# Kernel optimization log

Measured on AMD Instinct MI355X. Metric: run time of the kernel, lower is better.

## Reference

```python
import jax, jax.numpy as jnp
import numpy as np

HEAD_SIZE = 128
BLOCK_SIZE = 2048


def setup_inputs() -> dict:
    key = jax.random.key(0)
    k1, k2 = jax.random.split(key)
    B, T, D = 8, 2048, 1024
    x = jax.random.normal(k1, (B, T, D), dtype=jnp.float32)
    # Linear(dim, 3*head_size, bias=False): weight [3*head_size, dim], applied as x @ W.T
    W_qkv = jax.random.normal(k2, (3 * HEAD_SIZE, D), dtype=jnp.float32) * (1.0 / np.sqrt(D))
    return {"x": x, "W_qkv": W_qkv}


def reference(x, W_qkv):
    B, T, D = x.shape
    qkv = jnp.einsum('btd,hd->bth', x, W_qkv)  # [B, T, 3*head_size]
    q = qkv[:, :, :HEAD_SIZE]
    k = qkv[:, :, HEAD_SIZE:2 * HEAD_SIZE]
    v = qkv[:, :, 2 * HEAD_SIZE:]
    scale = 1.0 / np.sqrt(HEAD_SIZE).astype(np.float32)
    score = jnp.einsum('bqh,bkh->bqk', q, k) * scale  # [B, T, T]
    causal = jnp.tril(jnp.ones((T, T), dtype=bool))
    score = jnp.where(causal, score, -jnp.inf)
    attn = jax.nn.softmax(score, axis=-1)
    # dropout p=0.0 (eval) -> identity
    return jnp.einsum('bqk,bkh->bqh', attn, v)  # [B, T, head_size]
```

## Files before the change

kernel.cpp:

```cpp
#include <hip/hip_runtime.h>
#include <hip/hip_bf16.h>
#include <math.h>

#define D_MODEL 1024
#define TLEN    2048

typedef __attribute__((ext_vector_type(8))) short short8;
typedef __attribute__((ext_vector_type(4))) float f32x4;

static __device__ __forceinline__ unsigned short f2bf(float f) {
    __hip_bfloat16 h = __float2bfloat16(f);
    return __builtin_bit_cast(unsigned short, h);
}
static __device__ __forceinline__ float bf2f(unsigned short u) {
    unsigned int x = ((unsigned int)u) << 16;
    return __builtin_bit_cast(float, x);
}
static __device__ __forceinline__ void lds_cp16(void* lds, const void* g) {
    __builtin_amdgcn_global_load_lds(
        (const __attribute__((address_space(1))) unsigned int*)g,
        (__attribute__((address_space(3))) unsigned int*)lds, 16, 0, 0);
}

__global__ __launch_bounds__(256) void pack_w(const float* __restrict__ W,
                                              unsigned short* __restrict__ wt) {
    const int id = blockIdx.x * 256 + threadIdx.x;
    const int h  = id >> 7;
    const int kg = id & 127;
    const int k0 = kg * 8;
    const int kt = k0 >> 6;
    const int kin = k0 & 63;
    const float4 a = *(const float4*)&W[(size_t)h * D_MODEL + k0];
    const float4 b = *(const float4*)&W[(size_t)h * D_MODEL + k0 + 4];
    short8 v;
    v[0] = (short)f2bf(a.x); v[1] = (short)f2bf(a.y);
    v[2] = (short)f2bf(a.z); v[3] = (short)f2bf(a.w);
    v[4] = (short)f2bf(b.x); v[5] = (short)f2bf(b.y);
    v[6] = (short)f2bf(b.z); v[7] = (short)f2bf(b.w);
    const size_t dst = ((size_t)kt * 384 + h) * 64 + (kin ^ ((h & 7) * 8));
    *(short8*)&wt[dst] = v;
}

__global__ __launch_bounds__(256, 2) void qkv_gemm(const float* __restrict__ x,
                                                   const unsigned short* __restrict__ wt,
                                                   unsigned short* __restrict__ qk,
                                                   unsigned short* __restrict__ vt) {
    __shared__ unsigned short As[32 * 64];
    __shared__ unsigned short Bs[384 * 64];

    const int tid  = threadIdx.x;
    const int lane = tid & 63;
    const int w    = tid >> 6;
    const int cc   = lane & 15, g = lane >> 4;
    const int row0 = blockIdx.x * 32;

    const int xr  = tid >> 3;
    const int xg  = tid & 7;

    const f32x4 zero = {0.f, 0.f, 0.f, 0.f};
    f32x4 acc[2][6];
#pragma unroll
    for (int i = 0; i < 2; ++i)
#pragma unroll
        for (int j = 0; j < 6; ++j) acc[i][j] = zero;

    const float* xrow = x + (size_t)(row0 + xr) * D_MODEL + xg * 8;
    float4 xa0 = *(const float4*)(xrow);
    float4 xa1 = *(const float4*)(xrow + 4);

    const unsigned short* wsrc0 = wt + w * 6144 + lane * 8;
    unsigned short* bdst = Bs + w * 6144;

    const int aw = xr * 64 + ((xg ^ (xr & 7)) << 3);

    for (int kt = 0; kt < 16; ++kt) {
        __syncthreads();
        {
            short8 s0;
            s0[0] = (short)f2bf(xa0.x); s0[1] = (short)f2bf(xa0.y);
            s0[2] = (short)f2bf(xa0.z); s0[3] = (short)f2bf(xa0.w);
            s0[4] = (short)f2bf(xa1.x); s0[5] = (short)f2bf(xa1.y);
            s0[6] = (short)f2bf(xa1.z); s0[7] = (short)f2bf(xa1.w);
            *(short8*)&As[aw] = s0;
        }
        const unsigned short* wtk = wsrc0 + (size_t)kt * 24576;
#pragma unroll
        for (int i = 0; i < 12; ++i)
            lds_cp16(bdst + i * 512, wtk + i * 512);
        __syncthreads();

        short8 af[2][2], bf[2][6];
#pragma unroll
        for (int ks = 0; ks < 2; ++ks) {
#pragma unroll
            for (int mt = 0; mt < 2; ++mt) {
                const int row = mt * 16 + cc;
                af[ks][mt] = *(const short8*)&As[row * 64 + (((ks * 4 + g) ^ (row & 7)) << 3)];
            }
#pragma unroll
            for (int nt = 0; nt < 6; ++nt) {
                const int h = w * 96 + nt * 16 + cc;
                bf[ks][nt] = *(const short8*)&Bs[h * 64 + (((ks * 4 + g) ^ (h & 7)) << 3)];
            }
        }
        if (kt + 1 < 16) {
            xa0 = *(const float4*)(xrow + (kt + 1) * 64);
            xa1 = *(const float4*)(xrow + (kt + 1) * 64 + 4);
        }
        __builtin_amdgcn_s_setprio(1);
#pragma unroll
        for (int ks = 0; ks < 2; ++ks)
#pragma unroll
            for (int mt = 0; mt < 2; ++mt)
#pragma unroll
                for (int nt = 0; nt < 6; ++nt)
                    acc[mt][nt] = __builtin_amdgcn_mfma_f32_16x16x32_bf16(
                        af[ks][mt], bf[ks][nt], acc[mt][nt], 0, 0, 0);
        __builtin_amdgcn_s_setprio(0);
    }

    const int bb  = row0 >> 11;
    const int tr0 = row0 & 2047;
#pragma unroll
    for (int mt = 0; mt < 2; ++mt)
#pragma unroll
        for (int nt = 0; nt < 6; ++nt) {
            const int h = w * 96 + nt * 16 + cc;
            if (h < 256) {
                const float qs = (h < 128) ? 0.08838834764831845f : 1.0f;
#pragma unroll
                for (int r = 0; r < 4; ++r) {
                    const int row = row0 + mt * 16 + g * 4 + r;
                    qk[(size_t)row * 256 + h] = f2bf(acc[mt][nt][r] * qs);
                }
            } else {
                const int d    = h - 256;
                const int trow = tr0 + mt * 16 + g * 4;
                ushort4 u;
                u.x = f2bf(acc[mt][nt][0]);
                u.y = f2bf(acc[mt][nt][1]);
                u.z = f2bf(acc[mt][nt][2]);
                u.w = f2bf(acc[mt][nt][3]);
                *(ushort4*)&vt[((size_t)(bb * 128 + d)) * TLEN + trow] = u;
            }
        }
}

__global__ __launch_bounds__(256, 3) void attn_part(const unsigned short* __restrict__ qk,
                                                    const unsigned short* __restrict__ vt,
                                                    unsigned short* __restrict__ po,
                                                    float2* __restrict__ ml) {
    __shared__ unsigned short Ks[64 * 128];
    __shared__ unsigned short Vs[128 * 64];
    __shared__ unsigned short Ps[4][16][72];

    const int tid  = threadIdx.x;
    const int lane = tid & 63;
    const int w    = tid >> 6;
    const int cc   = lane & 15, g = lane >> 4;
    const int bx   = blockIdx.x;
    const int qt   = 31 - (bx / 3);
    const int ggg  = bx % 3;
    const int b    = blockIdx.y;
    const int q0   = qt * 64;
    const int slot = (b * 32 + qt) * 3 + ggg;
    const int n    = qt + 1;
    const int cnt  = (n > ggg) ? ((n - ggg + 2) / 3) : 0;

    if (cnt == 0) {
#pragma unroll
        for (int nt = 0; nt < 8; ++nt)
#pragma unroll
            for (int r = 0; r < 4; ++r)
                po[((size_t)slot * 64 + w * 16 + g * 4 + r) * 128 + nt * 16 + cc] = 0;
        if (g == 0) ml[slot * 64 + w * 16 + cc] = make_float2(-INFINITY, 0.f);
        return;
    }

    short8 qf[4];
    {
        const unsigned short* qb =
            qk + ((size_t)(b * TLEN + q0 + w * 16 + cc)) * 256 + g * 8;
#pragma unroll
        for (int kt = 0; kt < 4; ++kt) qf[kt] = *(const short8*)(qb + kt * 32);
    }

    const f32x4 zero = {0.f, 0.f, 0.f, 0.f};
    f32x4 o[8];
#pragma unroll
    for (int nt = 0; nt < 8; ++nt) o[nt] = zero;
    float mrun = -INFINITY, lrun = 0.f;

    int koff[4], voff[2];
#pragma unroll
    for (int kt = 0; kt < 4; ++kt)
        koff[kt] = cc * 128 + (((kt * 4 + g) ^ (cc & 7)) << 3);
#pragma unroll
    for (int ks = 0; ks < 2; ++ks)
        voff[ks] = cc * 64 + (((ks * 4 + g) ^ (cc & 7)) << 3);

    const int kRow = tid >> 2;
    const int kG0  = (tid & 3) * 4;
    const int vRow = tid >> 1;
    const int vG0  = (tid & 1) * 4;
    const unsigned short* kgp = qk + ((size_t)(b * TLEN + kRow)) * 256 + 128 + kG0 * 8;
    const unsigned short* vgp = vt + ((size_t)(b * 128 + vRow)) * TLEN + vG0 * 8;

    short8 kr[4], vr[4];
#pragma unroll
    for (int i = 0; i < 4; ++i) kr[i] = *(const short8*)(kgp + (size_t)ggg * 16384 + i * 8);
#pragma unroll
    for (int i = 0; i < 4; ++i) vr[i] = *(const short8*)(vgp + ggg * 64 + i * 8);

    for (int s = 0; s < cnt; ++s) {
        const int t  = 3 * s + ggg;
        const int j0 = t * 64;
        __syncthreads();
#pragma unroll
        for (int i = 0; i < 4; ++i) {
            *(short8*)&Ks[kRow * 128 + (((kG0 + i) ^ (kRow & 7)) << 3)] = kr[i];
            *(short8*)&Vs[vRow * 64  + (((vG0 + i) ^ (vRow & 7)) << 3)] = vr[i];
        }
        __syncthreads();
        if (s + 1 < cnt) {
            const int tn = t + 3;
#pragma unroll
            for (int i = 0; i < 4; ++i) kr[i] = *(const short8*)(kgp + (size_t)tn * 16384 + i * 8);
#pragma unroll
            for (int i = 0; i < 4; ++i) vr[i] = *(const short8*)(vgp + tn * 64 + i * 8);
        }

        f32x4 st[4];
#pragma unroll
        for (int jt = 0; jt < 4; ++jt) st[jt] = zero;
        __builtin_amdgcn_s_setprio(1);
#pragma unroll
        for (int kt = 0; kt < 4; ++kt)
#pragma unroll
            for (int jt = 0; jt < 4; ++jt) {
                const short8 kf = *(const short8*)&Ks[koff[kt] + jt * 2048];
                st[jt] = __builtin_amdgcn_mfma_f32_16x16x32_bf16(kf, qf[kt], st[jt], 0, 0, 0);
            }
        __builtin_amdgcn_s_setprio(0);

        if (t == qt) {
            const int qg = q0 + w * 16 + cc;
            const int jb = j0 + 4 * g;
#pragma unroll
            for (int jt = 0; jt < 4; ++jt)
#pragma unroll
                for (int r = 0; r < 4; ++r)
                    if (jb + jt * 16 + r > qg) st[jt][r] = -INFINITY;
        }
        float pmax = -INFINITY;
#pragma unroll
        for (int jt = 0; jt < 4; ++jt) {
            const float a = fmaxf(st[jt][0], st[jt][1]);
            const float c = fmaxf(st[jt][2], st[jt][3]);
            pmax = fmaxf(pmax, fmaxf(a, c));
        }
        pmax = fmaxf(pmax, __shfl_xor(pmax, 16));
        pmax = fmaxf(pmax, __shfl_xor(pmax, 32));

        if (!__all(pmax <= mrun + 8.f)) {
            const float newm  = fmaxf(mrun, pmax);
            const float alpha = __expf(mrun - newm);
            mrun = newm;
            lrun *= alpha;
            float arow[4];
#pragma unroll
            for (int r = 0; r < 4; ++r) arow[r] = __shfl(alpha, 20 * g + r);
#pragma unroll
            for (int nt = 0; nt < 8; ++nt)
#pragma unroll
                for (int r = 0; r < 4; ++r) o[nt][r] *= arow[r];
        }

        float rs = 0.f;
#pragma unroll
        for (int jt = 0; jt < 4; ++jt) {
            const float p0 = __expf(st[jt][0] - mrun);
            const float p1 = __expf(st[jt][1] - mrun);
            const float p2 = __expf(st[jt][2] - mrun);
            const float p3 = __expf(st[jt][3] - mrun);
            rs += (p0 + p1) + (p2 + p3);
            uint2 pw;
            pw.x = (unsigned int)f2bf(p0) | ((unsigned int)f2bf(p1) << 16);
            pw.y = (unsigned int)f2bf(p2) | ((unsigned int)f2bf(p3) << 16);
            *(uint2*)&Ps[w][cc][jt * 16 + 4 * g] = pw;
        }
        rs += __shfl_xor(rs, 16);
        rs += __shfl_xor(rs, 32);
        lrun += rs;

        asm volatile("s_waitcnt lgkmcnt(0)" ::: "memory");
        __builtin_amdgcn_sched_barrier(0);

        __builtin_amdgcn_s_setprio(1);
#pragma unroll
        for (int ks = 0; ks < 2; ++ks) {
            const short8 pa = *(const short8*)&Ps[w][cc][ks * 32 + g * 8];
#pragma unroll
            for (int nt = 0; nt < 8; ++nt) {
                const short8 vf = *(const short8*)&Vs[voff[ks] + nt * 1024];
                o[nt] = __builtin_amdgcn_mfma_f32_16x16x32_bf16(pa, vf, o[nt], 0, 0, 0);
            }
        }
        __builtin_amdgcn_s_setprio(0);
    }

#pragma unroll
    for (int nt = 0; nt < 8; ++nt)
#pragma unroll
        for (int r = 0; r < 4; ++r)
            po[((size_t)slot * 64 + w * 16 + g * 4 + r) * 128 + nt * 16 + cc] =
                f2bf(o[nt][r]);
    if (g == 0) ml[slot * 64 + w * 16 + cc] = make_float2(mrun, lrun);
}

__global__ __launch_bounds__(256) void attn_merge(const unsigned short* __restrict__ po,
                                                  const float2* __restrict__ ml,
                                                  float* __restrict__ out) {
    const int bq   = blockIdx.x;
    const int row  = threadIdx.x >> 2;
    const int cs   = (threadIdx.x & 3) * 32;
    const int slot = bq * 3;

    const float2 ml0 = ml[(size_t)(slot + 0) * 64 + row];
    const float2 ml1 = ml[(size_t)(slot + 1) * 64 + row];
    const float2 ml2 = ml[(size_t)(slot + 2) * 64 + row];
    const float M  = fmaxf(fmaxf(ml0.x, ml1.x), ml2.x);
    float e0 = __expf(ml0.x - M);
    float e1 = __expf(ml1.x - M);
    float e2 = __expf(ml2.x - M);
    const float inv = 1.f / (ml0.y * e0 + ml1.y * e1 + ml2.y * e2);
    e0 *= inv; e1 *= inv; e2 *= inv;

    const unsigned short* p0 = po + ((size_t)(slot + 0) * 64 + row) * 128 + cs;
    const unsigned short* p1 = po + ((size_t)(slot + 1) * 64 + row) * 128 + cs;
    const unsigned short* p2 = po + ((size_t)(slot + 2) * 64 + row) * 128 + cs;
    float* op = out + ((size_t)bq * 64 + row) * 128 + cs;

#pragma unroll
    for (int i = 0; i < 4; ++i) {
        const short8 a = *(const short8*)(p0 + i * 8);
        const short8 b = *(const short8*)(p1 + i * 8);
        const short8 c = *(const short8*)(p2 + i * 8);
        float4 o0, o1;
        o0.x = bf2f((unsigned short)a[0]) * e0 + bf2f((unsigned short)b[0]) * e1 + bf2f((unsigned short)c[0]) * e2;
        o0.y = bf2f((unsigned short)a[1]) * e0 + bf2f((unsigned short)b[1]) * e1 + bf2f((unsigned short)c[1]) * e2;
        o0.z = bf2f((unsigned short)a[2]) * e0 + bf2f((unsigned short)b[2]) * e1 + bf2f((unsigned short)c[2]) * e2;
        o0.w = bf2f((unsigned short)a[3]) * e0 + bf2f((unsigned short)b[3]) * e1 + bf2f((unsigned short)c[3]) * e2;
        o1.x = bf2f((unsigned short)a[4]) * e0 + bf2f((unsigned short)b[4]) * e1 + bf2f((unsigned short)c[4]) * e2;
        o1.y = bf2f((unsigned short)a[5]) * e0 + bf2f((unsigned short)b[5]) * e1 + bf2f((unsigned short)c[5]) * e2;
        o1.z = bf2f((unsigned short)a[6]) * e0 + bf2f((unsigned short)b[6]) * e1 + bf2f((unsigned short)c[6]) * e2;
        o1.w = bf2f((unsigned short)a[7]) * e0 + bf2f((unsigned short)b[7]) * e1 + bf2f((unsigned short)c[7]) * e2;
        *(float4*)(op + i * 8)     = o0;
        *(float4*)(op + i * 8 + 4) = o1;
    }
}

extern "C" void kernel_launch(void* const* d_in, const int* in_sizes, int n_in,
                              void* d_out, int out_size, void* d_ws, size_t ws_size,
                              hipStream_t stream) {
    (void)in_sizes; (void)n_in; (void)out_size; (void)ws_size;
    const float* x = (const float*)d_in[0];
    const float* W = (const float*)d_in[1];
    float* out = (float*)d_out;

    unsigned short* qkbf = (unsigned short*)d_ws;
    unsigned short* vtbf = qkbf + (size_t)16384 * 256;
    unsigned short* wtbf = vtbf + (size_t)8 * 128 * 2048;
    unsigned short* pobf = wtbf + (size_t)16 * 384 * 64;
    float2*         mlf  = (float2*)(pobf + (size_t)768 * 64 * 128);

    pack_w<<<dim3(192), 256, 0, stream>>>(W, wtbf);
    qkv_gemm<<<dim3(512), 256, 0, stream>>>(x, wtbf, qkbf, vtbf);
    attn_part<<<dim3(96, 8), 256, 0, stream>>>(qkbf, vtbf, pobf, mlf);
    attn_merge<<<dim3(256), 256, 0, stream>>>(pobf, mlf, out);
}
```

Baseline: 70.34 us.

## Double-buffer QKV GEMM tiles and enlarge block to 64 rows with 8 warps

```diff
diff --git a/kernel.cpp b/kernel.cpp
--- a/kernel.cpp
+++ b/kernel.cpp
@@ -41,21 +41,22 @@
     *(short8*)&wt[dst] = v;
 }
 
-__global__ __launch_bounds__(256, 2) void qkv_gemm(const float* __restrict__ x,
+__global__ __launch_bounds__(512, 1) void qkv_gemm(const float* __restrict__ x,
                                                    const unsigned short* __restrict__ wt,
                                                    unsigned short* __restrict__ qk,
                                                    unsigned short* __restrict__ vt) {
-    __shared__ unsigned short As[32 * 64];
-    __shared__ unsigned short Bs[384 * 64];
+    __shared__ unsigned short As[2][64 * 64];
+    __shared__ unsigned short Bs[2][384 * 64];
 
     const int tid  = threadIdx.x;
     const int lane = tid & 63;
     const int w    = tid >> 6;
+    const int wm   = w >> 2, wn = w & 3;
     const int cc   = lane & 15, g = lane >> 4;
-    const int row0 = blockIdx.x * 32;
-
-    const int xr  = tid >> 3;
-    const int xg  = tid & 7;
+    const int row0 = blockIdx.x * 64;
+
+    const int xr = tid >> 3;
+    const int xg = tid & 7;
 
     const f32x4 zero = {0.f, 0.f, 0.f, 0.f};
     f32x4 acc[2][6];
@@ -65,47 +66,58 @@
         for (int j = 0; j < 6; ++j) acc[i][j] = zero;
 
     const float* xrow = x + (size_t)(row0 + xr) * D_MODEL + xg * 8;
-    float4 xa0 = *(const float4*)(xrow);
-    float4 xa1 = *(const float4*)(xrow + 4);
-
-    const unsigned short* wsrc0 = wt + w * 6144 + lane * 8;
-    unsigned short* bdst = Bs + w * 6144;
-
     const int aw = xr * 64 + ((xg ^ (xr & 7)) << 3);
 
+    const unsigned short* wsrc = wt + w * 512 + lane * 8;
+
+    float4 xa0[2], xa1[2];
+    xa0[0] = *(const float4*)(xrow);
+    xa1[0] = *(const float4*)(xrow + 4);
+    xa0[1] = *(const float4*)(xrow + 64);
+    xa1[1] = *(const float4*)(xrow + 68);
+#pragma unroll
+    for (int i = 0; i < 6; ++i)
+        lds_cp16(&Bs[0][i * 4096 + w * 512], wsrc + i * 4096);
+
     for (int kt = 0; kt < 16; ++kt) {
+        const int cur = kt & 1;
+        {
+            const float4 a0 = xa0[cur], a1 = xa1[cur];
+            short8 s0;
+            s0[0] = (short)f2bf(a0.x); s0[1] = (short)f2bf(a0.y);
+            s0[2] = (short)f2bf(a0.z); s0[3] = (short)f2bf(a0.w);
+            s0[4] = (short)f2bf(a1.x); s0[5] = (short)f2bf(a1.y);
+            s0[6] = (short)f2bf(a1.z); s0[7] = (short)f2bf(a1.w);
+            *(short8*)&As[cur][aw] = s0;
+        }
         __syncthreads();
-        {
-            short8 s0;
-            s0[0] = (short)f2bf(xa0.x); s0[1] = (short)f2bf(xa0.y);
-            s0[2] = (short)f2bf(xa0.z); s0[3] = (short)f2bf(xa0.w);
-            s0[4] = (short)f2bf(xa1.x); s0[5] = (short)f2bf(xa1.y);
-            s0[6] = (short)f2bf(xa1.z); s0[7] = (short)f2bf(xa1.w);
-            *(short8*)&As[aw] = s0;
-        }
-        const unsigned short* wtk = wsrc0 + (size_t)kt * 24576;
-#pragma unroll
-        for (int i = 0; i < 12; ++i)
-            lds_cp16(bdst + i * 512, wtk + i * 512);
-        __syncthreads();
+
+        if (kt + 1 < 16) {
+            const unsigned short* wtk = wsrc + (size_t)(kt + 1) * 24576;
+#pragma unroll
+            for (int i = 0; i < 6; ++i)
+                lds_cp16(&Bs[cur ^ 1][i * 4096 + w * 512], wtk + i * 4096);
+        }
+        if (kt + 2 < 16) {
+            xa0[cur] = *(const float4*)(xrow + (kt + 2) * 64);
+            xa1[cur] = *(const float4*)(xrow + (kt + 2) * 64 + 4);
+        }
 
         short8 af[2][2], bf[2][6];
 #pragma unroll
         for (int ks = 0; ks < 2; ++ks) {
 #pragma unroll
             for (int mt = 0; mt < 2; ++mt) {
-                const int row = mt * 16 + cc;
-                af[ks][mt] = *(const short8*)&As[row * 64 + (((ks * 4 + g) ^ (row & 7)) << 3)];
+                const int row = wm * 32 + mt * 16 + cc;
+                af[ks][mt] = *(const short8*)
+                    &As[cur][row * 64 + (((ks * 4 + g) ^ (row & 7)) << 3)];
             }
 #pragma unroll
             for (int nt = 0; nt < 6; ++nt) {
-                const int h = w * 96 + nt * 16 + cc;
-                bf[ks][nt] = *(const short8*)&Bs[h * 64 + (((ks * 4 + g) ^ (h & 7)) << 3)];
-            }
-        }
-        if (kt + 1 < 16) {
-            xa0 = *(const float4*)(xrow + (kt + 1) * 64);
-            xa1 = *(const float4*)(xrow + (kt + 1) * 64 + 4);
+                const int h = wn * 96 + nt * 16 + cc;
+                bf[ks][nt] = *(const short8*)
+                    &Bs[cur][h * 64 + (((ks * 4 + g) ^ (h & 7)) << 3)];
+            }
         }
         __builtin_amdgcn_s_setprio(1);
 #pragma unroll
@@ -125,17 +137,17 @@
     for (int mt = 0; mt < 2; ++mt)
 #pragma unroll
         for (int nt = 0; nt < 6; ++nt) {
-            const int h = w * 96 + nt * 16 + cc;
+            const int h = wn * 96 + nt * 16 + cc;
             if (h < 256) {
                 const float qs = (h < 128) ? 0.08838834764831845f : 1.0f;
 #pragma unroll
                 for (int r = 0; r < 4; ++r) {
-                    const int row = row0 + mt * 16 + g * 4 + r;
+                    const int row = row0 + wm * 32 + mt * 16 + g * 4 + r;
                     qk[(size_t)row * 256 + h] = f2bf(acc[mt][nt][r] * qs);
                 }
             } else {
                 const int d    = h - 256;
-                const int trow = tr0 + mt * 16 + g * 4;
+                const int trow = tr0 + wm * 32 + mt * 16 + g * 4;
                 ushort4 u;
                 u.x = f2bf(acc[mt][nt][0]);
                 u.y = f2bf(acc[mt][nt][1]);
@@ -375,7 +387,7 @@
     float2*         mlf  = (float2*)(pobf + (size_t)768 * 64 * 128);
 
     pack_w<<<dim3(192), 256, 0, stream>>>(W, wtbf);
-    qkv_gemm<<<dim3(512), 256, 0, stream>>>(x, wtbf, qkbf, vtbf);
+    qkv_gemm<<<dim3(256), 512, 0, stream>>>(x, wtbf, qkbf, vtbf);
     attn_part<<<dim3(96, 8), 256, 0, stream>>>(qkbf, vtbf, pobf, mlf);
     attn_merge<<<dim3(256), 256, 0, stream>>>(pobf, mlf, out);
 }
```

Result: no change. 69.40 us (-1.3%).
